# Kernel optimization log

Hardware: AMD Instinct MI355X
Metric: run time of the kernel (lower is better)

The kernel has to match this reference:

```python
import jax, jax.numpy as jnp
import numpy as np

# dims
B, LP, CIN, AUX = 8, 1024, 64, 32
COUT, OUT_LEN = 64, 512
DM, DI, NS, PH, NH = 1024, 2048, 16, 64, 32  # d_model, d_inner, d_state, headdim, n_heads
NL, PATCH, KPRE, KCONV = 4, 8, 5, 4
GG, KH, CHUNK = 8, 2048, 64  # kan grid, kan hidden, chunk_size
DIN = 2 * DI + 2 * NS + NH   # in_proj output: z, xBC, dt
CONV_DIM = DI + 2 * NS


def _conv1d(x, w, b, stride, pad_l, pad_r, groups=1):
    # x: [B, C, L], w: [O, I/groups, K]
    y = jax.lax.conv_general_dilated(x, w, (stride,), [(pad_l, pad_r)],
                                     dimension_numbers=("NCH", "OIH", "NCH"),
                                     feature_group_count=groups)
    return y + b[None, :, None]


def _rmsnorm(x, w):
    return x * jax.lax.rsqrt(jnp.mean(x * x, axis=-1, keepdims=True) + 1e-5) * w


def _mamba(u, in_w, conv_w, conv_b, A_log, Dh, dt_bias, out_w):
    # Mamba2-style selective SSM block (bias-free projections, causal depthwise conv).
    Bs, L, _ = u.shape
    zxbcdt = jnp.einsum("bld,ed->ble", u, in_w)  # [B,L,DIN]
    z = zxbcdt[..., :DI]
    xBC = zxbcdt[..., DI:DI + CONV_DIM]
    dt = jax.nn.softplus(zxbcdt[..., DI + CONV_DIM:] + dt_bias)  # [B,L,NH]
    xBC = jax.nn.silu(_conv1d(xBC.transpose(0, 2, 1), conv_w, conv_b, 1, KCONV - 1, 0,
                              groups=CONV_DIM)).transpose(0, 2, 1)
    xh = xBC[..., :DI].reshape(Bs, L, NH, PH)
    Bm = xBC[..., DI:DI + NS]   # [B,L,NS]
    Cm = xBC[..., DI + NS:]     # [B,L,NS]
    dA = jnp.exp(-jnp.exp(A_log) * dt)  # [B,L,NH]

    def step(s, t):
        x_t, B_t, C_t, dA_t, dt_t = t
        s = s * dA_t[:, :, None, None] + jnp.einsum("bhp,bn,bh->bhpn", x_t, B_t, dt_t)
        return s, jnp.einsum("bhpn,bn->bhp", s, C_t)

    s0 = jnp.zeros((Bs, NH, PH, NS), u.dtype)
    xs = (xh.transpose(1, 0, 2, 3), Bm.transpose(1, 0, 2), Cm.transpose(1, 0, 2),
          dA.transpose(1, 0, 2), dt.transpose(1, 0, 2))
    _, ys = jax.lax.scan(step, s0, xs)  # ys: [L,B,NH,PH]
    y = ys.transpose(1, 0, 2, 3) + xh * Dh[None, None, :, None]
    y = y.reshape(Bs, L, DI) * jax.nn.silu(z)
    return jnp.einsum("ble,de->bld", y, out_w)


def _kan(x, log_bw, base_w, base_b, spline_w):
    # Gaussian-basis KAN layer: base Linear + spline Linear over RBF expansion.
    grid = jnp.linspace(-2.0, 2.0, GG)
    bw = jnp.exp(log_bw)[None] + 1e-6                 # [1,in,1]
    basis = jnp.exp(-((x[..., None] - grid[None, None, :]) ** 2) / (2.0 * bw * bw))
    return x @ base_w.T + base_b + basis.reshape(x.shape[0], -1) @ spline_w.T


def setup_inputs() -> dict:
    ks = iter(jax.random.split(jax.random.key(0), 64))
    nrm = lambda shape, s=0.02: jax.random.normal(next(ks), shape, jnp.float32) * s
    inp = {"x_prefix": jax.random.normal(next(ks), (B, LP, CIN), jnp.float32),
           "y_aux": jax.random.normal(next(ks), (B, AUX), jnp.float32),
           "pre_conv_w": nrm((DM, CIN, KPRE), 0.1), "pre_conv_b": jnp.zeros((DM,)),
           "patch_w": nrm((DM, DM, PATCH), 0.05), "patch_b": jnp.zeros((DM,))}
    for pre in ("fwd", "bwd"):
        inp[pre + "_norm_w"] = jnp.ones((NL, DM))
        inp[pre + "_in_w"] = nrm((NL, DIN, DM))
        inp[pre + "_conv_w"] = nrm((NL, CONV_DIM, 1, KCONV), 0.1)
        inp[pre + "_conv_b"] = jnp.zeros((NL, CONV_DIM))
        inp[pre + "_A_log"] = jnp.zeros((NL, NH))
        inp[pre + "_D"] = jnp.ones((NL, NH))
        inp[pre + "_dt_bias"] = nrm((NL, NH), 0.5)
        inp[pre + "_out_w"] = nrm((NL, DM, DI))
    inp.update(aux_w=nrm((DM, AUX)), aux_b=jnp.zeros((DM,)),
               kan1_log_bw=jnp.zeros((3 * DM, 1)), kan1_base_w=nrm((KH, 3 * DM)),
               kan1_base_b=jnp.zeros((KH,)), kan1_spline_w=nrm((KH, 3 * DM * GG), 0.005),
               kan2_log_bw=jnp.zeros((KH, 1)), kan2_base_w=nrm((DM, KH)),
               kan2_base_b=jnp.zeros((DM,)), kan2_spline_w=nrm((DM, KH * GG), 0.005),
               shared_w=nrm((DM, DM)), shared_b=jnp.zeros((DM,)),
               heads_w=nrm((COUT, OUT_LEN, DM)), heads_b=jnp.zeros((COUT, OUT_LEN)))
    return inp


def reference(x_prefix, y_aux, pre_conv_w, pre_conv_b, patch_w, patch_b,
              fwd_norm_w, fwd_in_w, fwd_conv_w, fwd_conv_b, fwd_A_log, fwd_D, fwd_dt_bias, fwd_out_w,
              bwd_norm_w, bwd_in_w, bwd_conv_w, bwd_conv_b, bwd_A_log, bwd_D, bwd_dt_bias, bwd_out_w,
              aux_w, aux_b, kan1_log_bw, kan1_base_w, kan1_base_b, kan1_spline_w,
              kan2_log_bw, kan2_base_w, kan2_base_b, kan2_spline_w,
              shared_w, shared_b, heads_w, heads_b):
    # encode_prefix
    x = jax.nn.silu(_conv1d(x_prefix.transpose(0, 2, 1), pre_conv_w, pre_conv_b, 1, KPRE // 2, KPRE // 2))
    x = _conv1d(x, patch_w, patch_b, PATCH, 0, 0).transpose(0, 2, 1)  # [B, 128, DM]
    rem = x.shape[1] % CHUNK
    if rem:
        x = jnp.pad(x, ((0, 0), (0, CHUNK - rem), (0, 0)))
    h_f, h_b = x, x[:, ::-1]
    for i in range(NL):
        h_f = h_f + _mamba(_rmsnorm(h_f, fwd_norm_w[i]), fwd_in_w[i], fwd_conv_w[i], fwd_conv_b[i],
                           fwd_A_log[i], fwd_D[i], fwd_dt_bias[i], fwd_out_w[i])
        h_b = h_b + _mamba(_rmsnorm(h_b, bwd_norm_w[i]), bwd_in_w[i], bwd_conv_w[i], bwd_conv_b[i],
                           bwd_A_log[i], bwd_D[i], bwd_dt_bias[i], bwd_out_w[i])
    ctx = jnp.concatenate([h_f.mean(1), h_b[:, ::-1].mean(1)], axis=-1)  # [B, 2*DM]
    # fusion + heads
    aux = jax.nn.silu(y_aux @ aux_w.T + aux_b)
    fused = jnp.concatenate([ctx, aux], axis=-1)  # [B, 3*DM]
    fused = jax.nn.silu(_kan(fused, kan1_log_bw, kan1_base_w, kan1_base_b, kan1_spline_w))
    fused = jax.nn.silu(_kan(fused, kan2_log_bw, kan2_base_w, kan2_base_b, kan2_spline_w))
    fused = jax.nn.silu(fused @ shared_w.T + shared_b)
    # all channel heads fused into one batched GEMM: [B, OUT_LEN, COUT]
    return jnp.einsum("bd,cld->blc", fused, heads_w) + heads_b.T[None]
```

## Files before the change

kernel.cpp:

```cpp
#include <hip/hip_runtime.h>
#include <hip/hip_bf16.h>
#include <math.h>

#define B_    8
#define LP_   1024
#define CIN_  64
#define DM_   1024
#define DI_   2048
#define NS_   16
#define PH_   64
#define NH_   32
#define NL_   4
#define GG_   8
#define KH_   2048
#define DIN_  4160
#define NPAD_ 4224
#define CONVD_ 2080
#define L_    128
#define R_    1024
#define OUTL_ 512
#define COUT_ 64

typedef __bf16 bf16x8 __attribute__((ext_vector_type(8)));
typedef float f32x4 __attribute__((ext_vector_type(4)));
typedef unsigned short ushort;

__device__ __forceinline__ float silu_f(float x) { return x / (1.0f + expf(-x)); }

__device__ __forceinline__ ushort f2bu(float x) {
    union { __hip_bfloat16 h; ushort u; } c; c.h = __float2bfloat16(x); return c.u;
}
__device__ __forceinline__ float bu2f(ushort u) {
    union { ushort u; __hip_bfloat16 h; } c; c.u = u; return __bfloat162float(c.h);
}

__device__ __forceinline__ void gload_lds16(const void* g, void* l) {
    __builtin_amdgcn_global_load_lds((const __attribute__((address_space(1))) unsigned int*)g,
                                     (__attribute__((address_space(3))) unsigned int*)l, 16, 0, 0);
}

__device__ __forceinline__ float merge2(float a, float b, int mask, int lane) {
    float x = (lane & mask) ? b : a;
    float y = (lane & mask) ? a : b;
    return x + __shfl_xor(y, mask);
}
__device__ __forceinline__ float reduce8(float* a, int lane) {
    float c0 = merge2(a[0], a[1], 1, lane);
    float c1 = merge2(a[2], a[3], 1, lane);
    float c2 = merge2(a[4], a[5], 1, lane);
    float c3 = merge2(a[6], a[7], 1, lane);
    float d0 = merge2(c0, c1, 2, lane);
    float d1 = merge2(c2, c3, 2, lane);
    float e  = merge2(d0, d1, 4, lane);
    e += __shfl_xor(e, 8);
    e += __shfl_xor(e, 16);
    e += __shfl_xor(e, 32);
    return e;
}

#define CVT_IN_T4  1081344
#define CVT_OUT_T4 524288
#define CVT_PER    1605632
#define CVT_TOT    12845056
#define PREP_W1 327680
#define PREP_W2 8388608
#define PREP_W3 2621440
#define PREP_TOT 11337728
__global__ __launch_bounds__(256) void k_cvt_prep(
    const float* __restrict__ in0, const float* __restrict__ in1,
    const float* __restrict__ o0, const float* __restrict__ o1,
    __hip_bfloat16* __restrict__ wBBa, __hip_bfloat16* __restrict__ wOBa,
    const float* __restrict__ pre_w, const float* __restrict__ patch_w, const float* __restrict__ xp,
    __hip_bfloat16* __restrict__ wpreT, __hip_bfloat16* __restrict__ wpatchT, __hip_bfloat16* __restrict__ Apre)
{
    int gi = blockIdx.x * 256 + threadIdx.x;
    if (gi < CVT_TOT) {
        int ld = gi / CVT_PER;
        int r = gi - ld * CVT_PER;
        int l = ld >> 1, d = ld & 1;
        const float* inw  = (d ? in1 : in0) + (size_t)l * DIN_ * DM_;
        const float* outw = (d ? o1 : o0) + (size_t)l * DM_ * DI_;
        if (r < CVT_IN_T4) {
            int idx = r * 4; int row = idx >> 10;
            __hip_bfloat16* dst = wBBa + (size_t)ld * NPAD_ * 1024 + idx;
            if (row < DIN_) {
                float4 v = *(const float4*)(inw + idx);
                dst[0] = __float2bfloat16(v.x); dst[1] = __float2bfloat16(v.y);
                dst[2] = __float2bfloat16(v.z); dst[3] = __float2bfloat16(v.w);
            } else {
                dst[0] = __float2bfloat16(0.f); dst[1] = __float2bfloat16(0.f);
                dst[2] = __float2bfloat16(0.f); dst[3] = __float2bfloat16(0.f);
            }
        } else {
            int idx = (r - CVT_IN_T4) * 4;
            __hip_bfloat16* dst = wOBa + (size_t)ld * 2048 * 1024 + idx;
            float4 v = *(const float4*)(outw + idx);
            dst[0] = __float2bfloat16(v.x); dst[1] = __float2bfloat16(v.y);
            dst[2] = __float2bfloat16(v.z); dst[3] = __float2bfloat16(v.w);
        }
        return;
    }
    int idx = gi - CVT_TOT;
    if (idx < PREP_W1) {
        int d = idx / 320, kk = idx % 320;
        int kp = kk >> 6, c = kk & 63;
        wpreT[idx] = __float2bfloat16(pre_w[(d * CIN_ + c) * 5 + kp]);
    } else if (idx < PREP_W1 + PREP_W2) {
        int i = idx - PREP_W1;
        int d = i >> 13, kk = i & 8191;
        int kp = kk >> 10, din = kk & 1023;
        wpatchT[i] = __float2bfloat16(patch_w[((size_t)d << 13) + din * 8 + kp]);
    } else if (idx < PREP_TOT) {
        int i = idx - PREP_W1 - PREP_W2;
        int kk = i % 320; int r = i / 320;
        int l = r & 1023, b = r >> 10;
        int kp = kk >> 6, c = kk & 63;
        int lp = l + kp - 2;
        float v = 0.f;
        if (lp >= 0 && lp < LP_) v = xp[((size_t)b * LP_ + lp) * CIN_ + c];
        Apre[i] = __float2bfloat16(v);
    }
}

template<int BM, int BN>
__global__ __launch_bounds__(512) void k_gemm_mfma(
    const ushort* __restrict__ A, const ushort* __restrict__ B,
    const float* __restrict__ bias,
    float* __restrict__ Cf, __hip_bfloat16* __restrict__ Cb,
    int Kc, int ldk, int ldc, int Nstore, int act, int nsplit,
    long sA, long sB, long sC)
{
    constexpr int BK = 64;
    constexpr int WM = 64, WN = 32;
    constexpr int MR = WM / 16, NR = WN / 16;
    constexpr int ACH = BM * 8, BCH = BN * 8;
    __shared__ ushort sAs[2][BM * BK];
    __shared__ ushort sBs[2][BN * BK];
    int tid = threadIdx.x;
    int lane = tid & 63, w = tid >> 6;
    int wr = w >> 2, wc = w & 3;
    int z = blockIdx.z;
    int dir = z / nsplit, ks = z - dir * nsplit;
    int kbase = ks * Kc;
    int m0 = blockIdx.y * BM, n0 = blockIdx.x * BN;
    const ushort* Az = A + (size_t)dir * sA + kbase;
    const ushort* Bz = B + (size_t)dir * sB + kbase;

    auto STAGE = [&](int buf, int k0) {
        #pragma unroll
        for (int c = tid; c < ACH; c += 512) {
            int row = c >> 3, gp = c & 7;
            int g = gp ^ (row & 7);
            gload_lds16(Az + (size_t)(m0 + row) * ldk + k0 + g * 8, (char*)&sAs[buf][0] + c * 16);
        }
        #pragma unroll
        for (int c = tid; c < BCH; c += 512) {
            int row = c >> 3, gp = c & 7;
            int g = gp ^ (row & 7);
            gload_lds16(Bz + (size_t)(n0 + row) * ldk + k0 + g * 8, (char*)&sBs[buf][0] + c * 16);
        }
    };

    f32x4 acc[MR][NR] = {};
    const int NT = Kc / BK;
    STAGE(0, 0);
    __syncthreads();
    int cur = 0;
    for (int t = 0; t < NT; ++t) {
        if (t + 1 < NT) STAGE(cur ^ 1, (t + 1) * BK);
        #pragma unroll
        for (int kk = 0; kk < 2; ++kk) {
            bf16x8 af[MR], bfr[NR];
            #pragma unroll
            for (int m = 0; m < MR; ++m) {
                int row = wr * WM + m * 16 + (lane & 15);
                int g = (kk * 4 + (lane >> 4)) ^ (lane & 7);
                af[m] = *(const bf16x8*)&sAs[cur][row * BK + g * 8];
            }
            #pragma unroll
            for (int n = 0; n < NR; ++n) {
                int row = wc * WN + n * 16 + (lane & 15);
                int g = (kk * 4 + (lane >> 4)) ^ (lane & 7);
                bfr[n] = *(const bf16x8*)&sBs[cur][row * BK + g * 8];
            }
            #pragma unroll
            for (int m = 0; m < MR; ++m)
                #pragma unroll
                for (int n = 0; n < NR; ++n)
                    acc[m][n] = __builtin_amdgcn_mfma_f32_16x16x32_bf16(af[m], bfr[n], acc[m][n], 0, 0, 0);
        }
        __syncthreads();
        cur ^= 1;
    }
    #pragma unroll
    for (int m = 0; m < MR; ++m) {
        int row = m0 + wr * WM + m * 16 + (lane >> 4) * 4;
        #pragma unroll
        for (int n = 0; n < NR; ++n) {
            int col = n0 + wc * WN + n * 16 + (lane & 15);
            if (col < Nstore) {
                if (act == 2) {
                    float* Cfz = Cf + (size_t)z * sC;
                    #pragma unroll
                    for (int j = 0; j < 4; ++j)
                        Cfz[(size_t)(row + j) * ldc + col] = acc[m][n][j];
                } else {
                    __hip_bfloat16* Cbz = Cb + (size_t)dir * sC;
                    float bv = bias ? bias[col] : 0.f;
                    #pragma unroll
                    for (int j = 0; j < 4; ++j) {
                        float v = acc[m][n][j] + bv;
                        if (act == 1) v = silu_f(v);
                        Cbz[(size_t)(row + j) * ldc + col] = __float2bfloat16(v);
                    }
                }
            }
        }
    }
}

__global__ __launch_bounds__(256) void k_patch_fin_rms(const float* __restrict__ part, const float* __restrict__ bias,
                                                       const float* __restrict__ w0, const float* __restrict__ w1,
                                                       float* __restrict__ hf, float* __restrict__ hb,
                                                       __hip_bfloat16* __restrict__ uB) {
    int r = blockIdx.x;
    int t = threadIdx.x;
    int c = t * 4;
    float4 o = *(const float4*)(bias + c);
    #pragma unroll
    for (int s = 0; s < 8; ++s) {
        float4 v = *(const float4*)(part + (size_t)s * 1048576 + ((size_t)r << 10) + c);
        o.x += v.x; o.y += v.y; o.z += v.z; o.w += v.w;
    }
    *(float4*)(hf + ((size_t)r << 10) + c) = o;
    int rb = r ^ 127;
    *(float4*)(hb + ((size_t)rb << 10) + c) = o;
    float ss = o.x * o.x + o.y * o.y + o.z * o.z + o.w * o.w;
    #pragma unroll
    for (int of = 32; of; of >>= 1) ss += __shfl_xor(ss, of);
    __shared__ float sred[4];
    if ((t & 63) == 0) sred[t >> 6] = ss;
    __syncthreads();
    float tot = sred[0] + sred[1] + sred[2] + sred[3];
    float scale = rsqrtf(tot * (1.0f / DM_) + 1e-5f);
    float4 wf = *(const float4*)(w0 + c);
    float4 wb = *(const float4*)(w1 + c);
    __hip_bfloat16* uf = uB + ((size_t)r << 10) + c;
    __hip_bfloat16* ub = uB + ((size_t)(1024 + rb) << 10) + c;
    uf[0] = __float2bfloat16(o.x * scale * wf.x); uf[1] = __float2bfloat16(o.y * scale * wf.y);
    uf[2] = __float2bfloat16(o.z * scale * wf.z); uf[3] = __float2bfloat16(o.w * scale * wf.w);
    ub[0] = __float2bfloat16(o.x * scale * wb.x); ub[1] = __float2bfloat16(o.y * scale * wb.y);
    ub[2] = __float2bfloat16(o.z * scale * wb.z); ub[3] = __float2bfloat16(o.w * scale * wb.w);
}

template<bool DO_RMS>
__global__ __launch_bounds__(256) void k_oproj_fin_rms(const float* __restrict__ part,
                                                       const float* __restrict__ w0, const float* __restrict__ w1,
                                                       float* __restrict__ h, __hip_bfloat16* __restrict__ uB) {
    int row = blockIdx.x;
    int t = threadIdx.x;
    int c = t * 4;
    const float* p = part + (size_t)(row >> 10) * 4194304 + (size_t)(row & 1023) * 1024 + c;
    float4 o = *(const float4*)(h + ((size_t)row << 10) + c);
    #pragma unroll
    for (int s = 0; s < 4; ++s) {
        float4 v = *(const float4*)(p + (size_t)s * 1048576);
        o.x += v.x; o.y += v.y; o.z += v.z; o.w += v.w;
    }
    *(float4*)(h + ((size_t)row << 10) + c) = o;
    if (DO_RMS) {
        float ss = o.x * o.x + o.y * o.y + o.z * o.z + o.w * o.w;
        #pragma unroll
        for (int of = 32; of; of >>= 1) ss += __shfl_xor(ss, of);
        __shared__ float sred[4];
        if ((t & 63) == 0) sred[t >> 6] = ss;
        __syncthreads();
        float tot = sred[0] + sred[1] + sred[2] + sred[3];
        float scale = rsqrtf(tot * (1.0f / DM_) + 1e-5f);
        const float* w = (row >> 10) ? w1 : w0;
        float4 wv = *(const float4*)(w + c);
        __hip_bfloat16* u = uB + ((size_t)row << 10) + c;
        u[0] = __float2bfloat16(o.x * scale * wv.x); u[1] = __float2bfloat16(o.y * scale * wv.y);
        u[2] = __float2bfloat16(o.z * scale * wv.z); u[3] = __float2bfloat16(o.w * scale * wv.w);
    }
}

__global__ __launch_bounds__(256) void k_scan(const __hip_bfloat16* __restrict__ zx,
                                              const float* __restrict__ cw0, const float* __restrict__ cw1,
                                              const float* __restrict__ cb0, const float* __restrict__ cb1,
                                              const float* __restrict__ dtb0, const float* __restrict__ dtb1,
                                              const float* __restrict__ al0, const float* __restrict__ al1,
                                              const float* __restrict__ D0, const float* __restrict__ D1,
                                              __hip_bfloat16* __restrict__ ys) {
    __shared__ float xs[L_ * PH_];
    __shared__ float Bsh[L_ * NS_];
    __shared__ float Csh[L_ * NS_];
    __shared__ float dts[L_];
    __shared__ float dAs[L_];
    int bx = blockIdx.x;
    int dir = bx >> 8, b = (bx >> 5) & 7, h = bx & 31;
    const __hip_bfloat16* zxd = zx + (size_t)dir * 1024 * DIN_;
    const float* cw = dir ? cw1 : cw0;
    const float* cb = dir ? cb1 : cb0;
    const float* dt_bias = dir ? dtb1 : dtb0;
    const float* A_log   = dir ? al1 : al0;
    const float* Dh      = dir ? D1 : D0;
    __hip_bfloat16* ysd  = ys + (size_t)dir * 1024 * DI_;
    int t = threadIdx.x;
    for (int i = t; i < 2048; i += 256) {
        int l = i >> 4, p4 = i & 15;
        int cc = h * PH_ + p4 * 4;
        float a0 = cb[cc + 0], a1 = cb[cc + 1], a2 = cb[cc + 2], a3 = cb[cc + 3];
        #pragma unroll
        for (int k = 0; k < 4; ++k) {
            int lp = l - 3 + k;
            if (lp >= 0) {
                ushort4 raw = *(const ushort4*)(zxd + (size_t)(b * L_ + lp) * DIN_ + DI_ + cc);
                a0 += bu2f(raw.x) * cw[(cc + 0) * 4 + k];
                a1 += bu2f(raw.y) * cw[(cc + 1) * 4 + k];
                a2 += bu2f(raw.z) * cw[(cc + 2) * 4 + k];
                a3 += bu2f(raw.w) * cw[(cc + 3) * 4 + k];
            }
        }
        float* xp = &xs[l * PH_ + p4 * 4];
        xp[0] = silu_f(a0); xp[1] = silu_f(a1); xp[2] = silu_f(a2); xp[3] = silu_f(a3);
    }
    for (int i = t; i < 1024; i += 256) {
        int l = i >> 3, q4 = i & 7;
        int cc = DI_ + q4 * 4;
        float a0 = cb[cc + 0], a1 = cb[cc + 1], a2 = cb[cc + 2], a3 = cb[cc + 3];
        #pragma unroll
        for (int k = 0; k < 4; ++k) {
            int lp = l - 3 + k;
            if (lp >= 0) {
                ushort4 raw = *(const ushort4*)(zxd + (size_t)(b * L_ + lp) * DIN_ + DI_ + cc);
                a0 += bu2f(raw.x) * cw[(cc + 0) * 4 + k];
                a1 += bu2f(raw.y) * cw[(cc + 1) * 4 + k];
                a2 += bu2f(raw.z) * cw[(cc + 2) * 4 + k];
                a3 += bu2f(raw.w) * cw[(cc + 3) * 4 + k];
            }
        }
        float r0 = silu_f(a0), r1 = silu_f(a1), r2 = silu_f(a2), r3 = silu_f(a3);
        if (q4 < 4) {
            float* bp = &Bsh[l * NS_ + q4 * 4];
            bp[0] = r0; bp[1] = r1; bp[2] = r2; bp[3] = r3;
        } else {
            float* cp = &Csh[l * NS_ + (q4 - 4) * 4];
            cp[0] = r0; cp[1] = r1; cp[2] = r2; cp[3] = r3;
        }
    }
    if (t < L_) {
        float v = bu2f(*(const ushort*)(zxd + (size_t)(b * L_ + t) * DIN_ + 4128 + h)) + dt_bias[h];
        float sp = v > 20.f ? v : log1pf(expf(v));
        dts[t] = sp;
        dAs[t] = expf(-expf(A_log[h]) * sp);
    }
    __syncthreads();
    int p = t >> 2, n0 = (t & 3) * 4;
    float Dv = Dh[h];
    float s0 = 0.f, s1 = 0.f, s2 = 0.f, s3 = 0.f;
    for (int l = 0; l < L_; ++l) {
        float x = xs[l * 64 + p];
        float dAv = dAs[l];
        float xdt = x * dts[l];
        s0 = s0 * dAv + xdt * Bsh[l * 16 + n0 + 0];
        s1 = s1 * dAv + xdt * Bsh[l * 16 + n0 + 1];
        s2 = s2 * dAv + xdt * Bsh[l * 16 + n0 + 2];
        s3 = s3 * dAv + xdt * Bsh[l * 16 + n0 + 3];
        float cp = s0 * Csh[l * 16 + n0 + 0] + s1 * Csh[l * 16 + n0 + 1]
                 + s2 * Csh[l * 16 + n0 + 2] + s3 * Csh[l * 16 + n0 + 3];
        cp += __shfl_xor(cp, 1);
        cp += __shfl_xor(cp, 2);
        if ((t & 3) == 0) xs[l * 64 + p] = cp + x * Dv;
    }
    __syncthreads();
    for (int i = t; i < L_ * PH_; i += 256) {
        int l = i >> 6, pp = i & 63;
        float z = bu2f(*(const ushort*)(zxd + (size_t)(b * L_ + l) * DIN_ + h * PH_ + pp));
        ysd[((size_t)(b * L_ + l)) * DI_ + h * PH_ + pp] = __float2bfloat16(xs[i] * silu_f(z));
    }
}

__device__ __forceinline__ void emit_basis(float v, float lbw, float* __restrict__ bas, size_t base) {
    float bw = expf(lbw) + 1e-6f;
    float inv = 1.0f / (2.0f * bw * bw);
    #pragma unroll
    for (int g = 0; g < GG_; ++g) {
        float gg = -2.0f + g * (4.0f / 7.0f);
        float df = v - gg;
        bas[base + g] = expf(-df * df * inv);
    }
}

__global__ __launch_bounds__(256) void k_meanctx_aux(const float* __restrict__ hf, const float* __restrict__ hb,
                                                     const float* __restrict__ y_aux, const float* __restrict__ aux_w,
                                                     const float* __restrict__ aux_b, const float* __restrict__ k1_lbw,
                                                     float* __restrict__ fused, float* __restrict__ bas1) {
    int bx = blockIdx.x;
    int t = threadIdx.x;
    if (bx < 64) {
        int b = bx >> 3, ch = bx & 7;
        int d4 = t & 31, lg = t >> 5;
        int d = ch * 128 + d4 * 4;
        float4 sf = {0,0,0,0}, sb = {0,0,0,0};
        for (int l = lg; l < L_; l += 8) {
            float4 a = *(const float4*)(hf + ((size_t)b * L_ + l) * DM_ + d);
            float4 c = *(const float4*)(hb + ((size_t)b * L_ + l) * DM_ + d);
            sf.x += a.x; sf.y += a.y; sf.z += a.z; sf.w += a.w;
            sb.x += c.x; sb.y += c.y; sb.z += c.z; sb.w += c.w;
        }
        __shared__ float rf[8][128], rb[8][128];
        *(float4*)&rf[lg][d4 * 4] = sf;
        *(float4*)&rb[lg][d4 * 4] = sb;
        __syncthreads();
        if (t < 128) {
            float s1 = 0.f, s2 = 0.f;
            #pragma unroll
            for (int g = 0; g < 8; ++g) { s1 += rf[g][t]; s2 += rb[g][t]; }
            s1 *= (1.f / L_); s2 *= (1.f / L_);
            int d1 = ch * 128 + t, d2 = DM_ + ch * 128 + t;
            fused[b * 3072 + d1] = s1;
            fused[b * 3072 + d2] = s2;
            emit_basis(s1, k1_lbw[d1], bas1, ((size_t)b * 3072 + d1) * GG_);
            emit_basis(s2, k1_lbw[d2], bas1, ((size_t)b * 3072 + d2) * GG_);
        }
    } else {
        int j = (bx - 64) * 256 + t;
        if (j >= DM_) return;
        for (int b = 0; b < B_; ++b) {
            float acc = aux_b[j];
            for (int a = 0; a < 32; ++a) acc += y_aux[b * 32 + a] * aux_w[j * 32 + a];
            float v = silu_f(acc);
            int d3 = 2 * DM_ + j;
            fused[b * 3072 + d3] = v;
            emit_basis(v, k1_lbw[d3], bas1, ((size_t)b * 3072 + d3) * GG_);
        }
    }
}

template<int MODE>
__global__ __launch_bounds__(256) void k_dotk(const float* __restrict__ Wsp, const float* __restrict__ Xsp, int Ksp,
                                              const float* __restrict__ Wb, const float* __restrict__ Xb, int Kb,
                                              const float* __restrict__ bias, float* __restrict__ out,
                                              int nsp, int nch, int Dout) {
    __shared__ float sX[8][1024];
    int ch = blockIdx.y;
    bool sp = (ch < nsp);
    const float* W = sp ? Wsp : Wb;
    const float* X = sp ? Xsp : Xb;
    int K = sp ? Ksp : Kb;
    int k0 = (sp ? ch : ch - nsp) * 1024;
    int tid = threadIdx.x;
    for (int i = tid; i < 2048; i += 256) {
        int b = i >> 8, kk = (i & 255) * 4;
        *(float4*)&sX[b][kk] = *(const float4*)(X + (size_t)b * K + k0 + kk);
    }
    __syncthreads();
    int wv = tid >> 6, lane = tid & 63;
    int rowBase = blockIdx.x * 32 + wv * 8;
    for (int j = 0; j < 8; ++j) {
        int row = rowBase + j;
        const float* wr = W + (size_t)row * K + k0;
        float acc[8] = {};
        #pragma unroll
        for (int it = 0; it < 4; ++it) {
            int k = it * 256 + lane * 4;
            float4 wvv = *(const float4*)(wr + k);
            #pragma unroll
            for (int b = 0; b < 8; ++b) {
                float4 xv = *(const float4*)&sX[b][k];
                acc[b] += wvv.x * xv.x + wvv.y * xv.y + wvv.z * xv.z + wvv.w * xv.w;
            }
        }
        float e = reduce8(acc, lane);
        if (lane < 8) {
            if (MODE == 0) {
                out[((size_t)row * nch + ch) * 8 + lane] = e;
            } else if (MODE == 1) {
                out[(size_t)lane * Dout + row] = silu_f(e + bias[row]);
            } else {
                int c = row >> 9, l = row & 511;
                out[((size_t)lane * OUTL_ + l) * COUT_ + c] = e + bias[row];
            }
        }
    }
}

__global__ __launch_bounds__(256) void k_fin1_basis2(const float* __restrict__ partial, const float* __restrict__ bb,
                                                     const float* __restrict__ k2_lbw,
                                                     float* __restrict__ k1, float* __restrict__ bas2) {
    int row = blockIdx.x * 256 + threadIdx.x;
    if (row >= 2048) return;
    float bbv = bb[row];
    float lb = expf(k2_lbw[row]) + 1e-6f;
    float inv = 1.0f / (2.0f * lb * lb);
    #pragma unroll
    for (int b = 0; b < 8; ++b) {
        float s = bbv;
        #pragma unroll
        for (int c = 0; c < 27; ++c) s += partial[((size_t)row * 27 + c) * 8 + b];
        float v = silu_f(s);
        k1[(size_t)b * 2048 + row] = v;
        #pragma unroll
        for (int g = 0; g < GG_; ++g) {
            float gg = -2.0f + g * (4.0f / 7.0f);
            float df = v - gg;
            bas2[((size_t)b * 2048 + row) * GG_ + g] = expf(-df * df * inv);
        }
    }
}

template<int NCH>
__global__ __launch_bounds__(256) void k_dot_fin(const float* __restrict__ partial, const float* __restrict__ base_b,
                                                 float* __restrict__ out, int Dout) {
    int row = blockIdx.x * 256 + threadIdx.x;
    if (row >= Dout) return;
    float bb = base_b[row];
    #pragma unroll
    for (int b = 0; b < 8; ++b) {
        float s = bb;
        #pragma unroll
        for (int c = 0; c < NCH; ++c) s += partial[((size_t)row * NCH + c) * 8 + b];
        out[(size_t)b * Dout + row] = silu_f(s);
    }
}

extern "C" void kernel_launch(void* const* d_in, const int* in_sizes, int n_in,
                              void* d_out, int out_size, void* d_ws, size_t ws_size,
                              hipStream_t stream) {
    const float* x_prefix = (const float*)d_in[0];
    const float* y_aux    = (const float*)d_in[1];
    const float* pre_w    = (const float*)d_in[2];
    const float* pre_b    = (const float*)d_in[3];
    const float* patch_w  = (const float*)d_in[4];
    const float* patch_b  = (const float*)d_in[5];
    const float* norm_w[2] = {(const float*)d_in[6],  (const float*)d_in[14]};
    const float* in_w[2]   = {(const float*)d_in[7],  (const float*)d_in[15]};
    const float* conv_w[2] = {(const float*)d_in[8],  (const float*)d_in[16]};
    const float* conv_b[2] = {(const float*)d_in[9],  (const float*)d_in[17]};
    const float* A_log[2]  = {(const float*)d_in[10], (const float*)d_in[18]};
    const float* Dvec[2]   = {(const float*)d_in[11], (const float*)d_in[19]};
    const float* dt_b[2]   = {(const float*)d_in[12], (const float*)d_in[20]};
    const float* out_w[2]  = {(const float*)d_in[13], (const float*)d_in[21]};
    const float* aux_w = (const float*)d_in[22];
    const float* aux_b = (const float*)d_in[23];
    const float* k1_lbw = (const float*)d_in[24];
    const float* k1_bw  = (const float*)d_in[25];
    const float* k1_bb  = (const float*)d_in[26];
    const float* k1_sw  = (const float*)d_in[27];
    const float* k2_lbw = (const float*)d_in[28];
    const float* k2_bw  = (const float*)d_in[29];
    const float* k2_bb  = (const float*)d_in[30];
    const float* k2_sw  = (const float*)d_in[31];
    const float* sh_w = (const float*)d_in[32];
    const float* sh_b = (const float*)d_in[33];
    const float* hw   = (const float*)d_in[34];
    const float* hbias= (const float*)d_in[35];
    float* ws = (float*)d_ws;
    float* out = (float*)d_out;

    const size_t o_ApreB   = 0;
    const size_t o_wpreTB  = 1310720;
    const size_t o_x1B     = 1474560;
    const size_t o_wpatchTB= 5668864;
    const size_t o_uB   = 0;
    const size_t o_zxB  = 1048576;
    const size_t o_ysB  = 5308416;
    const size_t o_hf   = 9863168;
    const size_t o_hb   = 10911744;
    const size_t o_wBBa = 11960320;
    const size_t o_wOBa = 29261824;
    const size_t o_spart= 37650432;
    const size_t total_f = 46039040;
    const size_t o_f1   = 0;
    const size_t o_bas1 = 24576;
    const size_t o_k1   = 221184;
    const size_t o_bas2 = 237568;
    const size_t o_k2   = 368640;
    const size_t o_f4   = 376832;
    const size_t o_part = 385024;
    if (ws_size < total_f * sizeof(float)) return;

    __hip_bfloat16* ApreB   = (__hip_bfloat16*)(ws + o_ApreB);
    __hip_bfloat16* wpreTB  = (__hip_bfloat16*)(ws + o_wpreTB);
    __hip_bfloat16* x1B     = (__hip_bfloat16*)(ws + o_x1B);
    __hip_bfloat16* wpatchTB= (__hip_bfloat16*)(ws + o_wpatchTB);
    __hip_bfloat16* uB      = (__hip_bfloat16*)(ws + o_uB);
    __hip_bfloat16* zxB     = (__hip_bfloat16*)(ws + o_zxB);
    __hip_bfloat16* ysB     = (__hip_bfloat16*)(ws + o_ysB);
    __hip_bfloat16* wBBa    = (__hip_bfloat16*)(ws + o_wBBa);
    __hip_bfloat16* wOBa    = (__hip_bfloat16*)(ws + o_wOBa);
    float* hf = ws + o_hf;
    float* hb = ws + o_hb;

    k_cvt_prep<<<(CVT_TOT + PREP_TOT + 255) / 256, 256, 0, stream>>>(
        in_w[0], in_w[1], out_w[0], out_w[1], wBBa, wOBa,
        pre_w, patch_w, x_prefix, wpreTB, wpatchTB, ApreB);
    k_gemm_mfma<128,128><<<dim3(8, 64, 1), 512, 0, stream>>>(
        (const ushort*)ApreB, (const ushort*)wpreTB, pre_b, nullptr, x1B,
        320, 320, 1024, 1024, 1, 1, 0, 0, 0);
    k_gemm_mfma<128,128><<<dim3(8, 8, 8), 512, 0, stream>>>(
        (const ushort*)x1B, (const ushort*)wpatchTB, nullptr, ws + o_spart, nullptr,
        1024, 8192, 1024, 1024, 2, 8, 0, 0, (long)1024 * 1024);
    k_patch_fin_rms<<<1024, 256, 0, stream>>>(ws + o_spart, patch_b, norm_w[0], norm_w[1], hf, hb, uB);

    for (int i = 0; i < NL_; ++i) {
        k_gemm_mfma<128,128><<<dim3(33, 8, 2), 512, 0, stream>>>(
            (const ushort*)uB, (const ushort*)(wBBa + (size_t)i * 2 * NPAD_ * 1024), nullptr, nullptr, zxB,
            1024, 1024, DIN_, DIN_, 0, 1, (long)1024 * 1024, (long)NPAD_ * 1024, (long)1024 * DIN_);
        k_scan<<<512, 256, 0, stream>>>(zxB,
            conv_w[0] + (size_t)i * CONVD_ * 4, conv_w[1] + (size_t)i * CONVD_ * 4,
            conv_b[0] + (size_t)i * CONVD_, conv_b[1] + (size_t)i * CONVD_,
            dt_b[0] + i * NH_, dt_b[1] + i * NH_, A_log[0] + i * NH_, A_log[1] + i * NH_,
            Dvec[0] + i * NH_, Dvec[1] + i * NH_, ysB);
        k_gemm_mfma<128,128><<<dim3(8, 8, 8), 512, 0, stream>>>(
            (const ushort*)ysB, (const ushort*)(wOBa + (size_t)i * 2 * 2048 * 1024), nullptr, ws + o_spart, nullptr,
            512, 2048, 1024, 1024, 2, 4, (long)1024 * 2048, (long)2048 * 1024, (long)1024 * 1024);
        if (i + 1 < NL_) {
            k_oproj_fin_rms<true><<<2048, 256, 0, stream>>>(ws + o_spart,
                norm_w[0] + (size_t)(i + 1) * DM_, norm_w[1] + (size_t)(i + 1) * DM_, hf, uB);
        } else {
            k_oproj_fin_rms<false><<<2048, 256, 0, stream>>>(ws + o_spart, nullptr, nullptr, hf, nullptr);
        }
    }

    k_meanctx_aux<<<68, 256, 0, stream>>>(hf, hb, y_aux, aux_w, aux_b, k1_lbw, ws + o_f1, ws + o_bas1);
    k_dotk<0><<<dim3(64, 27), 256, 0, stream>>>(k1_sw, ws + o_bas1, 24576, k1_bw, ws + o_f1, 3072,
                                                nullptr, ws + o_part, 24, 27, 2048);
    k_fin1_basis2<<<8, 256, 0, stream>>>(ws + o_part, k1_bb, k2_lbw, ws + o_k1, ws + o_bas2);
    k_dotk<0><<<dim3(32, 18), 256, 0, stream>>>(k2_sw, ws + o_bas2, 16384, k2_bw, ws + o_k1, 2048,
                                                nullptr, ws + o_part, 16, 18, 1024);
    k_dot_fin<18><<<4, 256, 0, stream>>>(ws + o_part, k2_bb, ws + o_k2, 1024);
    k_dotk<1><<<dim3(32, 1), 256, 0, stream>>>(nullptr, nullptr, 0, sh_w, ws + o_k2, 1024,
                                               sh_b, ws + o_f4, 0, 1, 1024);
    k_dotk<2><<<dim3(1024, 1), 256, 0, stream>>>(nullptr, nullptr, 0, hw, ws + o_f4, 1024,
                                                 hbias, out, 0, 1, 32768);
}
```

Measured before the change: 864.3 us.

## Halve GEMM K-tile, re-swizzle LDS, and remap workgroups across XCDs

Measured after the change: 836.3 us (median of 2 runs). 3.2% less time.

```diff
diff --git a/kernel.cpp b/kernel.cpp
--- a/kernel.cpp
+++ b/kernel.cpp
@@ -130,10 +130,10 @@
     int Kc, int ldk, int ldc, int Nstore, int act, int nsplit,
     long sA, long sB, long sC)
 {
-    constexpr int BK = 64;
+    constexpr int BK = 32;
     constexpr int WM = 64, WN = 32;
     constexpr int MR = WM / 16, NR = WN / 16;
-    constexpr int ACH = BM * 8, BCH = BN * 8;
+    constexpr int ACH = BM * 4, BCH = BN * 4;
     __shared__ ushort sAs[2][BM * BK];
     __shared__ ushort sBs[2][BN * BK];
     int tid = threadIdx.x;
@@ -142,24 +142,32 @@
     int z = blockIdx.z;
     int dir = z / nsplit, ks = z - dir * nsplit;
     int kbase = ks * Kc;
-    int m0 = blockIdx.y * BM, n0 = blockIdx.x * BN;
+    int H = blockIdx.y * gridDim.x + blockIdx.x;
+    int nwg = gridDim.x * gridDim.y;
+    int chunk = nwg >> 3;
+    int Lid = (H & 7) * chunk + (H >> 3);
+    int bx = Lid / gridDim.y;
+    int by = Lid - bx * gridDim.y;
+    int m0 = by * BM, n0 = bx * BN;
     const ushort* Az = A + (size_t)dir * sA + kbase;
     const ushort* Bz = B + (size_t)dir * sB + kbase;
 
     auto STAGE = [&](int buf, int k0) {
         #pragma unroll
         for (int c = tid; c < ACH; c += 512) {
-            int row = c >> 3, gp = c & 7;
-            int g = gp ^ (row & 7);
+            int row = c >> 2, gp = c & 3;
+            int g = gp ^ ((row >> 1) & 3);
             gload_lds16(Az + (size_t)(m0 + row) * ldk + k0 + g * 8, (char*)&sAs[buf][0] + c * 16);
         }
         #pragma unroll
         for (int c = tid; c < BCH; c += 512) {
-            int row = c >> 3, gp = c & 7;
-            int g = gp ^ (row & 7);
+            int row = c >> 2, gp = c & 3;
+            int g = gp ^ ((row >> 1) & 3);
             gload_lds16(Bz + (size_t)(n0 + row) * ldk + k0 + g * 8, (char*)&sBs[buf][0] + c * 16);
         }
     };
+
+    const int gsw = (((lane >> 4) ^ ((lane >> 1) & 3)) * 8);
 
     f32x4 acc[MR][NR] = {};
     const int NT = Kc / BK;
@@ -168,27 +176,18 @@
     int cur = 0;
     for (int t = 0; t < NT; ++t) {
         if (t + 1 < NT) STAGE(cur ^ 1, (t + 1) * BK);
-        #pragma unroll
-        for (int kk = 0; kk < 2; ++kk) {
-            bf16x8 af[MR], bfr[NR];
+        bf16x8 af[MR], bfr[NR];
+        #pragma unroll
+        for (int m = 0; m < MR; ++m)
+            af[m] = *(const bf16x8*)&sAs[cur][(wr * WM + m * 16 + (lane & 15)) * BK + gsw];
+        #pragma unroll
+        for (int n = 0; n < NR; ++n)
+            bfr[n] = *(const bf16x8*)&sBs[cur][(wc * WN + n * 16 + (lane & 15)) * BK + gsw];
+        #pragma unroll
+        for (int m = 0; m < MR; ++m)
             #pragma unroll
-            for (int m = 0; m < MR; ++m) {
-                int row = wr * WM + m * 16 + (lane & 15);
-                int g = (kk * 4 + (lane >> 4)) ^ (lane & 7);
-                af[m] = *(const bf16x8*)&sAs[cur][row * BK + g * 8];
-            }
-            #pragma unroll
-            for (int n = 0; n < NR; ++n) {
-                int row = wc * WN + n * 16 + (lane & 15);
-                int g = (kk * 4 + (lane >> 4)) ^ (lane & 7);
-                bfr[n] = *(const bf16x8*)&sBs[cur][row * BK + g * 8];
-            }
-            #pragma unroll
-            for (int m = 0; m < MR; ++m)
-                #pragma unroll
-                for (int n = 0; n < NR; ++n)
-                    acc[m][n] = __builtin_amdgcn_mfma_f32_16x16x32_bf16(af[m], bfr[n], acc[m][n], 0, 0, 0);
-        }
+            for (int n = 0; n < NR; ++n)
+                acc[m][n] = __builtin_amdgcn_mfma_f32_16x16x32_bf16(af[m], bfr[n], acc[m][n], 0, 0, 0);
         __syncthreads();
         cur ^= 1;
     }
```
